# Kernel tuning notes

Measured on AMD Instinct MI355X. Metric: run time of the kernel, lower is better.

The kernel has to match this reference:

```python
import jax, jax.numpy as jnp
import numpy as np

GS_ITERS = 10
GS_TAU = 0.5
NEG = -1e9
B, L, D, H = 4, 512, 64, 128


def gphi_scores(x, W1, b1, W2, b2):
    # Faithful to: concat([x_i, x_j]) -> Linear(2D,H) -> ReLU -> Linear(H,1).squeeze(-1)
    # Linear on the concat of [x_i, x_j] == x_i @ W1[:D] + x_j @ W1[D:] (fused, no [B,L,L,2D] tensor).
    d = x.shape[-1]
    pi = jnp.einsum('bld,dh->blh', x, W1[:d])   # row-index half of concat
    pj = jnp.einsum('bld,dh->blh', x, W1[d:])   # col-index half of concat
    h = jax.nn.relu(pi[:, :, None, :] + pj[:, None, :, :] + b1)  # [B,L,L,H]
    return jnp.einsum('blmh,h->blm', h, W2[:, 0]) + b2[0]        # [B,L,L]


def gumbel_sinkhorn(log_alpha, gumbel, pad_mask, tau, n_iters):
    # (scores + gumbel noise)/tau, mask padded rows/cols, alternate row/col log-normalization.
    la = (log_alpha + gumbel) / tau
    la = jnp.where(pad_mask, NEG, la)

    def step(la, _):
        la = la - jax.nn.logsumexp(la, axis=2, keepdims=True)  # row normalize
        la = la - jax.nn.logsumexp(la, axis=1, keepdims=True)  # col normalize
        la = jnp.where(pad_mask, NEG, la)
        return la, None

    la, _ = jax.lax.scan(step, la, None, length=n_iters)
    return jnp.exp(la)


def make_pad_mask(seq_lens, max_len):
    # mask_map logic: for a sequence of length s, rows < s have cols < s valid; rows >= s fully invalid.
    ar = jnp.arange(max_len)
    s = seq_lens[:, None, None]
    valid = (ar[None, :, None] < s) & (ar[None, None, :] < s)
    return ~valid  # True where gumbel-masked


def setup_inputs() -> dict:
    key = jax.random.key(0)
    ks = jax.random.split(key, 8)
    event_time = jax.random.uniform(ks[0], (B, L), dtype=jnp.float32) * 10.0
    event_type = jax.random.randint(ks[1], (B, L), 0, 50, dtype=jnp.int32)
    clean_enc_out = jax.random.normal(ks[2], (B, L, D), dtype=jnp.float32)
    seq_lens = jax.random.randint(ks[3], (B,), 1, L + 1, dtype=jnp.int32)
    u = jax.random.uniform(ks[4], (B, L, L), dtype=jnp.float32, minval=1e-6, maxval=1.0 - 1e-6)
    gumbel_noise = -jnp.log(-jnp.log(u))
    # gphi_mlp params (xavier-ish scaling)
    W1 = jax.random.normal(ks[5], (2 * D, H), dtype=jnp.float32) * (1.0 / np.sqrt(2 * D))
    b1 = jnp.full((H,), 0.01, dtype=jnp.float32)
    W2 = jax.random.normal(ks[6], (H, 1), dtype=jnp.float32) * (1.0 / np.sqrt(H))
    b2 = jnp.full((1,), 0.01, dtype=jnp.float32)
    return {"event_time": event_time, "event_type": event_type,
            "clean_enc_out": clean_enc_out, "seq_lens": seq_lens,
            "gumbel_noise": gumbel_noise, "W1": W1, "b1": b1, "W2": W2, "b2": b2}


def reference(event_time, event_type, clean_enc_out, seq_lens, gumbel_noise, W1, b1, W2, b2):
    pad_mask = make_pad_mask(seq_lens, event_time.shape[1])
    scores = gphi_scores(clean_enc_out, W1, b1, W2, b2)           # [B,L,L]
    perm = gumbel_sinkhorn(scores, gumbel_noise, pad_mask, GS_TAU, GS_ITERS)
    # same_perm_matrix=True, no_time_noise=True path
    types_permed = jnp.einsum('bl,blm->bm', event_type.astype(jnp.float32), perm)
    times_permed = jnp.einsum('bl,blm->bm', event_time, perm)
    return types_permed, times_permed, perm
```

## Files before the change

### kernel.cpp

```cpp
#include <hip/hip_runtime.h>
#include <cstdint>

#define BB 4
#define LL 512
#define DD 64
#define HH 128
#define NEGV -1000000000.0f
#define NBLK 256
#define NTHR 1024
#define NACT 64

union U8 { unsigned long long u; float2 f; };

__device__ __forceinline__ float2 cload_f2(const float* p) {
    U8 v;
    v.u = __hip_atomic_load((const unsigned long long*)p,
                            __ATOMIC_RELAXED, __HIP_MEMORY_SCOPE_AGENT);
    return v.f;
}
__device__ __forceinline__ void cstore_f2(float* p, float2 x) {
    U8 v; v.f = x;
    __hip_atomic_store((unsigned long long*)p, v.u,
                       __ATOMIC_RELAXED, __HIP_MEMORY_SCOPE_AGENT);
}

__device__ __forceinline__ void set_flag(unsigned* f) {
    __hip_atomic_store(f, 1u, __ATOMIC_RELAXED, __HIP_MEMORY_SCOPE_AGENT);
}
__device__ __forceinline__ void wait_flag(unsigned* f) {
    while (__hip_atomic_load(f, __ATOMIC_RELAXED, __HIP_MEMORY_SCOPE_AGENT) == 0u) {}
}

__device__ __forceinline__ float hmax4(float4 v) {
    return fmaxf(fmaxf(v.x, v.y), fmaxf(v.z, v.w));
}

#define FLG_GEMV 0
#define FLG_TILE 256
#define FLG_ITER 512
#define FLG_POUT 1152

__global__ __launch_bounds__(NTHR, 4) void mega(
    const float* __restrict__ etime, const int* __restrict__ etype,
    const float* __restrict__ x, const int* __restrict__ slens,
    const float* __restrict__ gum, const float* __restrict__ W1,
    const float* __restrict__ b1, const float* __restrict__ W2,
    const float* __restrict__ b2, float* __restrict__ out, float* __restrict__ ws)
{
    __shared__ float smem[19072];

    unsigned* flg = (unsigned*)ws;
    float* piG   = ws + 2048;
    float* pjG   = piG + BB * LL * HH;
    float* laG   = pjG + BB * LL * HH;
    float* cpkG  = laG + (size_t)BB * LL * LL;
    float* poutG = cpkG + (size_t)2 * BB * 16 * LL * 2;

    const int t = threadIdx.x;
    const int bx = blockIdx.x;

    {
        int arr = t >> 9;
        int row = (t >> 6) & 7;
        int h0  = (t & 63) << 1;
        int grow = (bx << 3) + row;
        const float* xr = x + (size_t)grow * DD;
        const float* wb = W1 + (size_t)(arr * DD) * HH + h0;
        float a0 = arr ? 0.f : b1[h0];
        float a1 = arr ? 0.f : b1[h0 + 1];
        #pragma unroll 8
        for (int d = 0; d < DD; ++d) {
            float xv = xr[d];
            float2 w = *(const float2*)(wb + d * HH);
            a0 = fmaf(xv, w.x, a0);
            a1 = fmaf(xv, w.y, a1);
        }
        cstore_f2((arr ? pjG : piG) + (size_t)grow * HH + h0, make_float2(a0, a1));
        __builtin_amdgcn_fence(__ATOMIC_RELEASE, "workgroup");
        __syncthreads();
        if (t == 0) set_flag(flg + FLG_GEMV + bx);
    }

    {
        float* sp  = smem;
        float* sq  = smem + 8192;
        float* sw2 = smem + 18944;
        int jt = bx & 7, it8 = (bx >> 3) & 7, b = bx >> 6;
        int i0 = it8 << 6, j0 = jt << 6;
        int rowb = b * LL + i0, colb = b * LL + j0;

        if (t < 8)              wait_flag(flg + FLG_GEMV + (b << 6) + (it8 << 3) + t);
        else if (t < 16)        wait_flag(flg + FLG_GEMV + (b << 6) + (jt << 3) + (t - 8));
        if (t < HH) sw2[t] = W2[t];
        __syncthreads();

        #pragma unroll
        for (int k = 0; k < 8; ++k) {
            int idx = (k << 10) + t;
            int buf = idx >> 12;
            int u   = idx & 4095;
            int row = u >> 6;
            int du  = u & 63;
            int q   = du >> 1;
            int hi  = du & 1;
            int dq  = q ^ ((row >> 2) & 7);
            const float* src = (buf ? pjG + (size_t)(colb + row) * HH
                                    : piG + (size_t)(rowb + row) * HH) + (du << 1);
            float2 v = cload_f2(src);
            float* dst = (buf ? sq : sp) + row * HH + (dq << 2) + (hi << 1);
            *(float2*)dst = v;
        }
        __syncthreads();

        int hg = t >> 8, tt = t & 255;
        int w = tt >> 6, lane = tt & 63;
        int ti = ((w >> 1) << 3) + (lane >> 3);
        int tj = ((w & 1) << 3) + (lane & 7);
        int kti = ti & 7, ktj = tj & 7;

        float acc[4][4];
        #pragma unroll
        for (int a = 0; a < 4; ++a)
            #pragma unroll
            for (int c = 0; c < 4; ++c) acc[a][c] = 0.f;

        for (int hq = hg * 8; hq < hg * 8 + 8; ++hq) {
            float4 w4 = *(const float4*)(sw2 + (hq << 2));
            int offi = (hq ^ kti) << 2;
            int offj = (hq ^ ktj) << 2;
            float4 pa[4], pb[4];
            #pragma unroll
            for (int a = 0; a < 4; ++a) pa[a] = *(const float4*)(sp + (4*ti + a) * HH + offi);
            #pragma unroll
            for (int c = 0; c < 4; ++c) pb[c] = *(const float4*)(sq + (4*tj + c) * HH + offj);
            #pragma unroll
            for (int a = 0; a < 4; ++a) {
                #pragma unroll
                for (int c = 0; c < 4; ++c) {
                    float t0 = fmaxf(pa[a].x + pb[c].x, 0.f);
                    float t1 = fmaxf(pa[a].y + pb[c].y, 0.f);
                    float t2 = fmaxf(pa[a].z + pb[c].z, 0.f);
                    float t3 = fmaxf(pa[a].w + pb[c].w, 0.f);
                    float s = acc[a][c];
                    s += t0 * w4.x; s += t1 * w4.y; s += t2 * w4.z; s += t3 * w4.w;
                    acc[a][c] = s;
                }
            }
        }
        __syncthreads();
        float* cbuf = smem;
        #pragma unroll
        for (int a = 0; a < 4; ++a)
            #pragma unroll
            for (int c = 0; c < 4; ++c)
                cbuf[(((hg << 8) + tt) << 4) + (a << 2) + c] = acc[a][c];
        __syncthreads();

        int tt2 = t >> 2, a2 = t & 3;
        int w2_ = tt2 >> 6, lane2 = tt2 & 63;
        int ti2 = ((w2_ >> 1) << 3) + (lane2 >> 3);
        int tj2 = ((w2_ & 1) << 3) + (lane2 & 7);
        float4 o = make_float4(0.f, 0.f, 0.f, 0.f);
        #pragma unroll
        for (int g = 0; g < 4; ++g) {
            float4 pp = *(const float4*)(cbuf + (((g << 8) + tt2) << 4) + (a2 << 2));
            o.x += pp.x; o.y += pp.y; o.z += pp.z; o.w += pp.w;
        }
        int sl = slens[b];
        float bb2 = b2[0];
        int ig = i0 + 4 * ti2 + a2;
        int jb = j0 + 4 * tj2;
        float4 g4 = *(const float4*)(gum + ((size_t)(b * LL + ig)) * LL + jb);
        bool iv = ig < sl;
        float4 res;
        res.x = (iv && (jb + 0) < sl) ? (o.x + bb2 + g4.x) * 2.0f : NEGV;
        res.y = (iv && (jb + 1) < sl) ? (o.y + bb2 + g4.y) * 2.0f : NEGV;
        res.z = (iv && (jb + 2) < sl) ? (o.z + bb2 + g4.z) * 2.0f : NEGV;
        res.w = (iv && (jb + 3) < sl) ? (o.w + bb2 + g4.w) * 2.0f : NEGV;
        float* lap = laG + ((size_t)(b * LL + ig)) * LL + jb;
        cstore_f2(lap,     make_float2(res.x, res.y));
        cstore_f2(lap + 2, make_float2(res.z, res.w));
        __builtin_amdgcn_fence(__ATOMIC_RELEASE, "workgroup");
        __syncthreads();
        if (t == 0) set_flag(flg + FLG_TILE + (b << 6) + (it8 << 3) + jt);
    }

    if (bx >= NACT) return;

    const int b2i = bx >> 4;
    const int stripe = bx & 15;
    const int r0 = stripe << 5;
    float* sla  = smem;
    float* redm = smem + 16384;
    float* reds = smem + 17408;
    float* clse = smem + 18432;
    const int sl_a = slens[b2i];
    float tyv = 0.f, tmv = 0.f;

    {
        if (t < 8) wait_flag(flg + FLG_TILE + (b2i << 6) + ((stripe >> 1) << 3) + t);
        __syncthreads();
        const float* src = laG + (((size_t)(b2i << 9) + r0) << 9);
        #pragma unroll
        for (int k = 0; k < 8; ++k) {
            int u = (k << 10) + t;
            float2 v = cload_f2(src + (u << 1));
            *(float2*)(sla + (u << 1)) = v;
        }
        if (t < 512) clse[t] = 0.f;
        __syncthreads();
    }

    for (int it = 0; it < 10; ++it) {
        const int par = it & 1;
        const int last = (it == 9);
        {
            int r = t >> 5, cq = t & 31;
            int grow = r0 + r;
            bool ivR = grow < sl_a;
            float4 v[4];
            #pragma unroll
            for (int k = 0; k < 4; ++k) {
                int cb = (cq + (k << 5)) << 2;
                float4 a = *(float4*)(sla + (r << 9) + cb);
                float4 l = *(const float4*)(clse + cb);
                v[k].x = (ivR && (cb + 0) < sl_a) ? a.x - l.x : NEGV;
                v[k].y = (ivR && (cb + 1) < sl_a) ? a.y - l.y : NEGV;
                v[k].z = (ivR && (cb + 2) < sl_a) ? a.z - l.z : NEGV;
                v[k].w = (ivR && (cb + 3) < sl_a) ? a.w - l.w : NEGV;
            }
            float m = fmaxf(fmaxf(hmax4(v[0]), hmax4(v[1])), fmaxf(hmax4(v[2]), hmax4(v[3])));
            #pragma unroll
            for (int off = 16; off; off >>= 1) m = fmaxf(m, __shfl_xor(m, off));
            float s = 0.f;
            #pragma unroll
            for (int k = 0; k < 4; ++k)
                s += __expf(v[k].x - m) + __expf(v[k].y - m) + __expf(v[k].z - m) + __expf(v[k].w - m);
            #pragma unroll
            for (int off = 16; off; off >>= 1) s += __shfl_xor(s, off);
            float lse = m + __logf(s);
            #pragma unroll
            for (int k = 0; k < 4; ++k) {
                v[k].x -= lse; v[k].y -= lse; v[k].z -= lse; v[k].w -= lse;
                *(float4*)(sla + (r << 9) + ((cq + (k << 5)) << 2)) = v[k];
            }
            __syncthreads();

            int c = t & 511, half = t >> 9;
            float vv[16];
            #pragma unroll
            for (int rr = 0; rr < 16; ++rr) vv[rr] = sla[(((half << 4) + rr) << 9) + c];
            float mp = vv[0];
            #pragma unroll
            for (int rr = 1; rr < 16; ++rr) mp = fmaxf(mp, vv[rr]);
            float spv = 0.f;
            #pragma unroll
            for (int rr = 0; rr < 16; ++rr) spv += __expf(vv[rr] - mp);
            redm[(half << 9) + c] = mp;
            reds[(half << 9) + c] = spv;
            __syncthreads();
            if (half == 0) {
                float m1 = redm[512 + c], s1 = reds[512 + c];
                float M = fmaxf(mp, m1);
                float S = fmaf(spv, __expf(mp - M), s1 * __expf(m1 - M));
                cstore_f2(cpkG + (size_t)(((((par * BB) + b2i) << 4) + stripe) * LL + c) * 2,
                          make_float2(M, S));
            }
            __builtin_amdgcn_fence(__ATOMIC_RELEASE, "workgroup");
            __syncthreads();
            if (t == 0) set_flag(flg + FLG_ITER + (((b2i * 10) + it) << 4) + stripe);
            if (t < 16) wait_flag(flg + FLG_ITER + (((b2i * 10) + it) << 4) + t);
            __syncthreads();
        }
        {
            if (t < 512) {
                const float* pB = cpkG + (size_t)((((par * BB) + b2i) << 4) * LL) * 2;
                float mreg[16], sreg[16];
                #pragma unroll
                for (int g = 0; g < 16; ++g) {
                    float2 ms = cload_f2(pB + (size_t)(g * LL + t) * 2);
                    mreg[g] = ms.x; sreg[g] = ms.y;
                }
                float M = mreg[0];
                #pragma unroll
                for (int g = 1; g < 16; ++g) M = fmaxf(M, mreg[g]);
                float S = 0.f;
                #pragma unroll
                for (int g = 0; g < 16; ++g)
                    S = fmaf(sreg[g], __expf(mreg[g] - M), S);
                clse[t] = M + __logf(S);
            }
            __syncthreads();

            if (last) {
                int r = t >> 5, cq = t & 31;
                int grow = r0 + r;
                bool ivR = grow < sl_a;
                float etf = (float)etype[(b2i << 9) + grow];
                float etv = etime[(b2i << 9) + grow];
                float4 p[4];
                #pragma unroll
                for (int k = 0; k < 4; ++k) {
                    int cb = (cq + (k << 5)) << 2;
                    float4 v = *(float4*)(sla + (r << 9) + cb);
                    float4 l = *(const float4*)(clse + cb);
                    float4 q;
                    q.x = (ivR && (cb + 0) < sl_a) ? __expf(v.x - l.x) : 0.f;
                    q.y = (ivR && (cb + 1) < sl_a) ? __expf(v.y - l.y) : 0.f;
                    q.z = (ivR && (cb + 2) < sl_a) ? __expf(v.z - l.z) : 0.f;
                    q.w = (ivR && (cb + 3) < sl_a) ? __expf(v.w - l.w) : 0.f;
                    p[k] = q;
                    *(float4*)(out + 2 * BB * LL + (((size_t)(b2i << 9) + grow) << 9) + cb) = q;
                }
                #pragma unroll
                for (int k = 0; k < 4; ++k) {
                    int cb = (cq + (k << 5)) << 2;
                    *(float4*)(sla + (r << 9) + cb) =
                        make_float4(p[k].x * etf, p[k].y * etf, p[k].z * etf, p[k].w * etf);
                }
                __syncthreads();
                {
                    int c2 = t & 511, h2 = t >> 9;
                    float sA = 0.f;
                    #pragma unroll
                    for (int rr = 0; rr < 16; ++rr) sA += sla[(((h2 << 4) + rr) << 9) + c2];
                    redm[(h2 << 9) + c2] = sA;
                }
                __syncthreads();
                if (t < 512) tyv = redm[t] + redm[512 + t];
                __syncthreads();
                #pragma unroll
                for (int k = 0; k < 4; ++k) {
                    int cb = (cq + (k << 5)) << 2;
                    *(float4*)(sla + (r << 9) + cb) =
                        make_float4(p[k].x * etv, p[k].y * etv, p[k].z * etv, p[k].w * etv);
                }
                __syncthreads();
                {
                    int c2 = t & 511, h2 = t >> 9;
                    float sB = 0.f;
                    #pragma unroll
                    for (int rr = 0; rr < 16; ++rr) sB += sla[(((h2 << 4) + rr) << 9) + c2];
                    reds[(h2 << 9) + c2] = sB;
                }
                __syncthreads();
                if (t < 512) {
                    tmv = reds[t] + reds[512 + t];
                    cstore_f2(poutG + (size_t)(((b2i << 4) + stripe) * LL + t) * 2,
                              make_float2(tyv, tmv));
                }
                __builtin_amdgcn_fence(__ATOMIC_RELEASE, "workgroup");
                __syncthreads();
                if (t == 0) set_flag(flg + FLG_POUT + (b2i << 4) + stripe);
            }
        }
    }

    if (t < 16) wait_flag(flg + FLG_POUT + (b2i << 4) + t);
    __syncthreads();
    if (t < 32) {
        int c = (stripe << 5) + t;
        float a = 0.f, d = 0.f;
        #pragma unroll
        for (int s = 0; s < 16; ++s) {
            float2 p = cload_f2(poutG + (size_t)(((b2i << 4) + s) * LL + c) * 2);
            a += p.x; d += p.y;
        }
        out[(b2i << 9) + c] = a;
        out[BB * LL + (b2i << 9) + c] = d;
    }
}

extern "C" void kernel_launch(void* const* d_in, const int* in_sizes, int n_in,
                              void* d_out, int out_size, void* d_ws, size_t ws_size,
                              hipStream_t stream)
{
    const float* etime = (const float*)d_in[0];
    const int*   etype = (const int*)d_in[1];
    const float* x     = (const float*)d_in[2];
    const int*   slens = (const int*)d_in[3];
    const float* gum   = (const float*)d_in[4];
    const float* W1    = (const float*)d_in[5];
    const float* b1    = (const float*)d_in[6];
    const float* W2    = (const float*)d_in[7];
    const float* b2    = (const float*)d_in[8];
    float* out = (float*)d_out;
    float* wsf = (float*)d_ws;

    hipMemsetAsync(d_ws, 0, 8192, stream);

    void* args[] = {(void*)&etime, (void*)&etype, (void*)&x, (void*)&slens, (void*)&gum,
                    (void*)&W1, (void*)&b1, (void*)&W2, (void*)&b2, (void*)&out, (void*)&wsf};
    hipError_t err = hipLaunchCooperativeKernel((const void*)mega, dim3(NBLK), dim3(NTHR),
                                                args, 0, stream);
    if (err != hipSuccess) {
        mega<<<NBLK, NTHR, 0, stream>>>(etime, etype, x, slens, gum, W1, b1, W2, b2, out, wsf);
    }
}
```

Before: 112.8 us.

## Replace per-iteration flag barrier with sign-tagged data polling for column partials

Drops the separate per-iteration flag barrier between the 16 stripe blocks of a batch. Each block now writes its (max, sum) column partial with a sign that alternates every two iterations. Readers spin directly on the partial data until every sign matches the expected parity, so the flag set/wait round-trip and one __syncthreads are removed. The column partial reduction is also collapsed to 512 threads over 32 rows instead of two halves plus a shared-memory merge. The cost is a larger memset to zero the partial buffer, and correctness now depends on the sign encoding, double-buffered slots, and relaxed-atomic ordering of the 8-byte stores.

Measured after the change: 133.7 us. 18.5% more time.

```diff
diff --git a/kernel.cpp b/kernel.cpp
--- a/kernel.cpp
+++ b/kernel.cpp
@@ -37,8 +37,7 @@
 
 #define FLG_GEMV 0
 #define FLG_TILE 256
-#define FLG_ITER 512
-#define FLG_POUT 1152
+#define FLG_POUT 512
 
 __global__ __launch_bounds__(NTHR, 4) void mega(
     const float* __restrict__ etime, const int* __restrict__ etype,
@@ -50,11 +49,11 @@
     __shared__ float smem[19072];
 
     unsigned* flg = (unsigned*)ws;
-    float* piG   = ws + 2048;
+    float* cpkG  = ws + 2048;
+    float* piG   = cpkG + 2 * BB * 16 * LL * 2;
     float* pjG   = piG + BB * LL * HH;
     float* laG   = pjG + BB * LL * HH;
-    float* cpkG  = laG + (size_t)BB * LL * LL;
-    float* poutG = cpkG + (size_t)2 * BB * 16 * LL * 2;
+    float* poutG = laG + (size_t)BB * LL * LL;
 
     const int t = threadIdx.x;
     const int bx = blockIdx.x;
@@ -212,8 +211,10 @@
     }
 
     for (int it = 0; it < 10; ++it) {
-        const int par = it & 1;
         const int last = (it == 9);
+        const int slot = it & 1;
+        const bool neg = (it >> 1) & 1;
+
         {
             int r = t >> 5, cq = t & 31;
             int grow = r0 + r;
@@ -244,115 +245,112 @@
                 v[k].x -= lse; v[k].y -= lse; v[k].z -= lse; v[k].w -= lse;
                 *(float4*)(sla + (r << 9) + ((cq + (k << 5)) << 2)) = v[k];
             }
-            __syncthreads();
-
-            int c = t & 511, half = t >> 9;
-            float vv[16];
-            #pragma unroll
-            for (int rr = 0; rr < 16; ++rr) vv[rr] = sla[(((half << 4) + rr) << 9) + c];
-            float mp = vv[0];
-            #pragma unroll
-            for (int rr = 1; rr < 16; ++rr) mp = fmaxf(mp, vv[rr]);
+        }
+        __syncthreads();
+
+        if (t < 512) {
+            float mp = sla[t];
+            #pragma unroll
+            for (int rr = 1; rr < 32; ++rr) mp = fmaxf(mp, sla[(rr << 9) + t]);
             float spv = 0.f;
             #pragma unroll
-            for (int rr = 0; rr < 16; ++rr) spv += __expf(vv[rr] - mp);
-            redm[(half << 9) + c] = mp;
-            reds[(half << 9) + c] = spv;
-            __syncthreads();
-            if (half == 0) {
-                float m1 = redm[512 + c], s1 = reds[512 + c];
-                float M = fmaxf(mp, m1);
-                float S = fmaf(spv, __expf(mp - M), s1 * __expf(m1 - M));
-                cstore_f2(cpkG + (size_t)(((((par * BB) + b2i) << 4) + stripe) * LL + c) * 2,
-                          make_float2(M, S));
+            for (int rr = 0; rr < 32; ++rr) spv += __expf(sla[(rr << 9) + t] - mp);
+            cstore_f2(cpkG + ((size_t)(((slot * BB + b2i) << 4) + stripe) * LL + t) * 2,
+                      make_float2(mp, neg ? -spv : spv));
+
+            const float* pB = cpkG + (size_t)(((slot * BB + b2i) << 4) * LL) * 2;
+            float mreg[16], sreg[16];
+            #pragma unroll
+            for (int g = 0; g < 16; ++g) {
+                float2 ms = cload_f2(pB + ((size_t)(g * LL + t)) * 2);
+                mreg[g] = ms.x; sreg[g] = ms.y;
+            }
+            while (true) {
+                bool ok = true;
+                #pragma unroll
+                for (int g = 0; g < 16; ++g)
+                    ok &= neg ? (sreg[g] < 0.f) : (sreg[g] > 0.f);
+                if (ok) break;
+                #pragma unroll
+                for (int g = 0; g < 16; ++g) {
+                    bool good = neg ? (sreg[g] < 0.f) : (sreg[g] > 0.f);
+                    if (!good) {
+                        float2 ms = cload_f2(pB + ((size_t)(g * LL + t)) * 2);
+                        mreg[g] = ms.x; sreg[g] = ms.y;
+                    }
+                }
+            }
+            float M = mreg[0];
+            #pragma unroll
+            for (int g = 1; g < 16; ++g) M = fmaxf(M, mreg[g]);
+            float S = 0.f;
+            #pragma unroll
+            for (int g = 0; g < 16; ++g)
+                S = fmaf(fabsf(sreg[g]), __expf(mreg[g] - M), S);
+            clse[t] = M + __logf(S);
+        }
+        __syncthreads();
+
+        if (last) {
+            int r = t >> 5, cq = t & 31;
+            int grow = r0 + r;
+            bool ivR = grow < sl_a;
+            float etf = (float)etype[(b2i << 9) + grow];
+            float etv = etime[(b2i << 9) + grow];
+            float4 p[4];
+            #pragma unroll
+            for (int k = 0; k < 4; ++k) {
+                int cb = (cq + (k << 5)) << 2;
+                float4 v = *(float4*)(sla + (r << 9) + cb);
+                float4 l = *(const float4*)(clse + cb);
+                float4 q;
+                q.x = (ivR && (cb + 0) < sl_a) ? __expf(v.x - l.x) : 0.f;
+                q.y = (ivR && (cb + 1) < sl_a) ? __expf(v.y - l.y) : 0.f;
+                q.z = (ivR && (cb + 2) < sl_a) ? __expf(v.z - l.z) : 0.f;
+                q.w = (ivR && (cb + 3) < sl_a) ? __expf(v.w - l.w) : 0.f;
+                p[k] = q;
+                *(float4*)(out + 2 * BB * LL + (((size_t)(b2i << 9) + grow) << 9) + cb) = q;
+            }
+            #pragma unroll
+            for (int k = 0; k < 4; ++k) {
+                int cb = (cq + (k << 5)) << 2;
+                *(float4*)(sla + (r << 9) + cb) =
+                    make_float4(p[k].x * etf, p[k].y * etf, p[k].z * etf, p[k].w * etf);
+            }
+            __syncthreads();
+            {
+                int c2 = t & 511, h2 = t >> 9;
+                float sA = 0.f;
+                #pragma unroll
+                for (int rr = 0; rr < 16; ++rr) sA += sla[(((h2 << 4) + rr) << 9) + c2];
+                redm[(h2 << 9) + c2] = sA;
+            }
+            __syncthreads();
+            if (t < 512) tyv = redm[t] + redm[512 + t];
+            __syncthreads();
+            #pragma unroll
+            for (int k = 0; k < 4; ++k) {
+                int cb = (cq + (k << 5)) << 2;
+                *(float4*)(sla + (r << 9) + cb) =
+                    make_float4(p[k].x * etv, p[k].y * etv, p[k].z * etv, p[k].w * etv);
+            }
+            __syncthreads();
+            {
+                int c2 = t & 511, h2 = t >> 9;
+                float sB = 0.f;
+                #pragma unroll
+                for (int rr = 0; rr < 16; ++rr) sB += sla[(((h2 << 4) + rr) << 9) + c2];
+                reds[(h2 << 9) + c2] = sB;
+            }
+            __syncthreads();
+            if (t < 512) {
+                tmv = reds[t] + reds[512 + t];
+                cstore_f2(poutG + (size_t)(((b2i << 4) + stripe) * LL + t) * 2,
+                          make_float2(tyv, tmv));
             }
             __builtin_amdgcn_fence(__ATOMIC_RELEASE, "workgroup");
             __syncthreads();
-            if (t == 0) set_flag(flg + FLG_ITER + (((b2i * 10) + it) << 4) + stripe);
-            if (t < 16) wait_flag(flg + FLG_ITER + (((b2i * 10) + it) << 4) + t);
-            __syncthreads();
-        }
-        {
-            if (t < 512) {
-                const float* pB = cpkG + (size_t)((((par * BB) + b2i) << 4) * LL) * 2;
-                float mreg[16], sreg[16];
-                #pragma unroll
-                for (int g = 0; g < 16; ++g) {
-                    float2 ms = cload_f2(pB + (size_t)(g * LL + t) * 2);
-                    mreg[g] = ms.x; sreg[g] = ms.y;
-                }
-                float M = mreg[0];
-                #pragma unroll
-                for (int g = 1; g < 16; ++g) M = fmaxf(M, mreg[g]);
-                float S = 0.f;
-                #pragma unroll
-                for (int g = 0; g < 16; ++g)
-                    S = fmaf(sreg[g], __expf(mreg[g] - M), S);
-                clse[t] = M + __logf(S);
-            }
-            __syncthreads();
-
-            if (last) {
-                int r = t >> 5, cq = t & 31;
-                int grow = r0 + r;
-                bool ivR = grow < sl_a;
-                float etf = (float)etype[(b2i << 9) + grow];
-                float etv = etime[(b2i << 9) + grow];
-                float4 p[4];
-                #pragma unroll
-                for (int k = 0; k < 4; ++k) {
-                    int cb = (cq + (k << 5)) << 2;
-                    float4 v = *(float4*)(sla + (r << 9) + cb);
-                    float4 l = *(const float4*)(clse + cb);
-                    float4 q;
-                    q.x = (ivR && (cb + 0) < sl_a) ? __expf(v.x - l.x) : 0.f;
-                    q.y = (ivR && (cb + 1) < sl_a) ? __expf(v.y - l.y) : 0.f;
-                    q.z = (ivR && (cb + 2) < sl_a) ? __expf(v.z - l.z) : 0.f;
-                    q.w = (ivR && (cb + 3) < sl_a) ? __expf(v.w - l.w) : 0.f;
-                    p[k] = q;
-                    *(float4*)(out + 2 * BB * LL + (((size_t)(b2i << 9) + grow) << 9) + cb) = q;
-                }
-                #pragma unroll
-                for (int k = 0; k < 4; ++k) {
-                    int cb = (cq + (k << 5)) << 2;
-                    *(float4*)(sla + (r << 9) + cb) =
-                        make_float4(p[k].x * etf, p[k].y * etf, p[k].z * etf, p[k].w * etf);
-                }
-                __syncthreads();
-                {
-                    int c2 = t & 511, h2 = t >> 9;
-                    float sA = 0.f;
-                    #pragma unroll
-                    for (int rr = 0; rr < 16; ++rr) sA += sla[(((h2 << 4) + rr) << 9) + c2];
-                    redm[(h2 << 9) + c2] = sA;
-                }
-                __syncthreads();
-                if (t < 512) tyv = redm[t] + redm[512 + t];
-                __syncthreads();
-                #pragma unroll
-                for (int k = 0; k < 4; ++k) {
-                    int cb = (cq + (k << 5)) << 2;
-                    *(float4*)(sla + (r << 9) + cb) =
-                        make_float4(p[k].x * etv, p[k].y * etv, p[k].z * etv, p[k].w * etv);
-                }
-                __syncthreads();
-                {
-                    int c2 = t & 511, h2 = t >> 9;
-                    float sB = 0.f;
-                    #pragma unroll
-                    for (int rr = 0; rr < 16; ++rr) sB += sla[(((h2 << 4) + rr) << 9) + c2];
-                    reds[(h2 << 9) + c2] = sB;
-                }
-                __syncthreads();
-                if (t < 512) {
-                    tmv = reds[t] + reds[512 + t];
-                    cstore_f2(poutG + (size_t)(((b2i << 4) + stripe) * LL + t) * 2,
-                              make_float2(tyv, tmv));
-                }
-                __builtin_amdgcn_fence(__ATOMIC_RELEASE, "workgroup");
-                __syncthreads();
-                if (t == 0) set_flag(flg + FLG_POUT + (b2i << 4) + stripe);
-            }
+            if (t == 0) set_flag(flg + FLG_POUT + (b2i << 4) + stripe);
         }
     }
 
@@ -387,7 +385,7 @@
     float* out = (float*)d_out;
     float* wsf = (float*)d_ws;
 
-    hipMemsetAsync(d_ws, 0, 8192, stream);
+    hipMemsetAsync(d_ws, 0, 8192 + 2 * BB * 16 * LL * 2 * sizeof(float), stream);
 
     void* args[] = {(void*)&etime, (void*)&etype, (void*)&x, (void*)&slens, (void*)&gum,
                     (void*)&W1, (void*)&b1, (void*)&W2, (void*)&b2, (void*)&out, (void*)&wsf};
```
